# Optimization experiments

Hardware: AMD Instinct MI355X
Metric: run time of the kernel (lower is better)

Reference implementation:

```python
import jax, jax.numpy as jnp
import numpy as np

PRED_LEN = 6

def conv2d_same(x, w):
    # x: (B,H,W,Cin), w: (kh,kw,Cin,Cout) -> (B,H,W,Cout)
    return jax.lax.conv_general_dilated(
        x, w, window_strides=(1, 1), padding='SAME',
        dimension_numbers=('NHWC', 'HWIO', 'NHWC'))

def setup_inputs() -> dict:
    key = jax.random.key(0)
    ks = jax.random.split(key, 6)
    B, T, H, W, C = 8, 12, 128, 128, 1
    F = 64
    s_in = 1.0 / np.sqrt(3 * 3 * C)
    s_rec = 1.0 / np.sqrt(3 * 3 * F)
    return {
        'x': jax.random.normal(ks[0], (B, T, H, W, C), jnp.float32),
        'kernel': jax.random.normal(ks[1], (3, 3, C, 4 * F), jnp.float32) * s_in,
        'rec_kernel': jax.random.normal(ks[2], (3, 3, F, 4 * F), jnp.float32) * s_rec,
        'bias': jnp.zeros((4 * F,), jnp.float32),
        'w_out': jax.random.normal(ks[3], (3, 3, F, 1), jnp.float32) * s_rec,
        'b_out': jnp.zeros((1,), jnp.float32),
        'w_proj': jax.random.normal(ks[4], (1, 1, 1, F), jnp.float32),
        'b_proj': jnp.zeros((F,), jnp.float32),
    }

def reference(x, kernel, rec_kernel, bias, w_out, b_out, w_proj, b_proj):
    B, T, H, W, C = x.shape
    F = rec_kernel.shape[2]

    def step(carry, xt):
        h, c = carry
        # fused gate pre-activations: (B,H,W,4F), Keras gate order i,f,g,o
        z = conv2d_same(xt, kernel) + conv2d_same(h, rec_kernel) + bias
        i, f, g, o = jnp.split(z, 4, axis=-1)
        c_new = jax.nn.sigmoid(f) * c + jax.nn.sigmoid(i) * jnp.tanh(g)
        h_new = jax.nn.sigmoid(o) * jnp.tanh(c_new)
        return (h_new, c_new), None

    h0 = jnp.zeros((B, H, W, F), x.dtype)
    c0 = jnp.zeros((B, H, W, F), x.dtype)
    (h, c), _ = jax.lax.scan(step, (h0, c0), jnp.moveaxis(x, 1, 0))

    preds = []
    cur = h
    for _ in range(PRED_LEN):
        pred = jax.nn.sigmoid(conv2d_same(cur, w_out) + b_out)  # (B,H,W,1)
        preds.append(pred)
        cur = jax.nn.relu(conv2d_same(pred, w_proj) + b_proj)   # (B,H,W,F)
    return jnp.stack(preds, axis=1)  # (B,PRED_LEN,H,W,1)
```

## Files before the change

### kernel.cpp

```cpp
#include <hip/hip_runtime.h>
#include <math.h>

#define BB 8
#define TT 12
#define HH 128
#define WW 128
#define FF 64
#define GG 256
#define PRED_LEN 6
#define TW 64
#define TWD 32

typedef __attribute__((ext_vector_type(8))) short short8;
typedef __attribute__((ext_vector_type(4))) float floatx4;

__device__ __forceinline__ float sigf(float x) { return 1.f / (1.f + __expf(-x)); }
__device__ __forceinline__ float tanhfast(float x) { return 1.f - 2.f / (__expf(2.f * x) + 1.f); }

__device__ __forceinline__ unsigned short f2bf(float x) {
    unsigned u = __float_as_uint(x);
    u = (u + 0x7FFFu + ((u >> 16) & 1u)) >> 16;
    return (unsigned short)u;
}

__device__ __forceinline__ void decode_step(int wg, int& b, int& y, int& x0) {
    int lin = (wg & 7) * 128 + (wg >> 3);
    b = lin >> 7;
    int rem = lin & 127;
    y = (rem >> 1) * 2;
    x0 = (rem & 1) * TW;
}

__device__ __forceinline__ void decode_dec(int wg, int& b, int& y, int& x0) {
    int lin = (wg & 7) * 512 + (wg >> 3);
    b = lin >> 9;
    int rem = lin & 511;
    y = rem >> 2;
    x0 = (rem & 3) * TWD;
}

__global__ __launch_bounds__(256) void pack_wr(
    const float* __restrict__ wr, const float* __restrict__ wk,
    const float* __restrict__ bias, short8* __restrict__ packed)
{
    int e = blockIdx.x * 256 + threadIdx.x;
    if (e >= 19 * 16 * 64) return;
    int lane = e & 63;
    int rest = e >> 6;
    int nt = rest & 15;
    int ch = rest >> 4;
    int col = lane & 15, kpart = lane >> 4;
    int n = nt * 16 + col;
    short8 v;
    if (ch < 18) {
        int kc = ch & 1, tap = ch >> 1;
        #pragma unroll
        for (int j = 0; j < 8; ++j) {
            int k = kc * 32 + kpart * 8 + j;
            v[j] = (short)f2bf(wr[((size_t)(tap * 64 + k)) * GG + n]);
        }
    } else {
        #pragma unroll
        for (int j = 0; j < 8; ++j) {
            int k = kpart * 8 + j;
            unsigned short r = 0;
            if (k < 9) r = f2bf(wk[k * GG + n]);
            else if (k == 9) r = f2bf(bias[n]);
            v[j] = (short)r;
        }
    }
    packed[e] = v;
}

template<bool FIRST>
__global__ __launch_bounds__(512, 4) void lstm_step_mfma(
    const float* __restrict__ x,
    int t,
    const unsigned short* __restrict__ h_in,
    float* __restrict__ c_buf,
    unsigned short* __restrict__ h_out,
    const short8* __restrict__ packedB)
{
    __shared__ __align__(16) unsigned short sh[4 * 66 * FF];
    __shared__ __align__(16) unsigned short sxa[2][TW * 32];
    __shared__ float sx[4][66];

    const int tid = threadIdx.x;
    int b, y, x0;
    decode_step(blockIdx.x, b, y, x0);
    char* shb = (char*)sh;

    if (!FIRST) {
        for (int i = tid; i < 4 * 66 * 8; i += 512) {
            int cq  = i & 7;
            int rc  = i >> 3;
            int col = rc % 66, r = rc / 66;
            int gy = y + r - 1, gx = x0 + col - 1;
            uint4 v = make_uint4(0u, 0u, 0u, 0u);
            if ((unsigned)gy < HH && (unsigned)gx < WW)
                v = *(const uint4*)(h_in + ((((size_t)b * HH + gy) * WW + gx) * FF + cq * 8));
            int byte = ((r * 66 + col) * FF + cq * 8) * 2;
            byte ^= ((col & 7) << 4);
            *(uint4*)(shb + byte) = v;
        }
    }
    for (int i = tid; i < 4 * 66; i += 512) {
        int col = i % 66, r = i / 66;
        int gy = y + r - 1, gx = x0 + col - 1;
        float v = 0.f;
        if ((unsigned)gy < HH && (unsigned)gx < WW)
            v = x[(((size_t)b * TT + t) * HH + gy) * WW + gx];
        sx[r][col] = v;
    }
    __syncthreads();

    {
        int rr  = tid >> 8;
        int t2  = tid & 255;
        int px  = t2 >> 2, kpc = t2 & 3;
        short8 v;
        #pragma unroll
        for (int j = 0; j < 8; ++j) {
            int k = kpc * 8 + j;
            unsigned short r = 0;
            if (k < 9) r = f2bf(sx[rr + k / 3][px + (k % 3)]);
            else if (k == 9) r = (unsigned short)0x3F80;
            v[j] = (short)r;
        }
        int byte = (px * 64 + kpc * 16) ^ ((px & 7) << 4);
        *(short8*)((char*)sxa[rr] + byte) = v;
    }
    __syncthreads();

    const int l    = tid & 63;
    const int w    = tid >> 6;
    const int sw   = w & 3;
    const int rrow = w >> 2;
    const int lc = l & 15;
    const int kp = l >> 4;
    const int gcol = sw * 16 + lc;

    floatx4 acc[4][4];
    #pragma unroll
    for (int m = 0; m < 4; ++m)
        #pragma unroll
        for (int q = 0; q < 4; ++q)
            acc[m][q] = (floatx4){0.f, 0.f, 0.f, 0.f};

    if (!FIRST) {
        #pragma unroll
        for (int c = 0; c < 18; ++c) {
            const int tap_ = c >> 1, kc_ = c & 1, dy_ = tap_ / 3, dx_ = tap_ % 3;
            short8 af[4], bf[4];
            #pragma unroll
            for (int m_ = 0; m_ < 4; ++m_) {
                const int col_ = m_ * 16 + lc + dx_;
                int byte_ = (((dy_ + rrow) * 66 + col_) * FF + kc_ * 32 + kp * 8) * 2;
                byte_ ^= ((col_ & 7) << 4);
                af[m_] = *(const short8*)(shb + byte_);
            }
            #pragma unroll
            for (int q_ = 0; q_ < 4; ++q_)
                bf[q_] = packedB[(size_t)(c * 16 + (q_ * 4 + sw)) * 64 + l];
            #pragma unroll
            for (int m_ = 0; m_ < 4; ++m_)
                #pragma unroll
                for (int q_ = 0; q_ < 4; ++q_)
                    acc[m_][q_] = __builtin_amdgcn_mfma_f32_16x16x32_bf16(
                        af[m_], bf[q_], acc[m_][q_], 0, 0, 0);
        }
    }
    {
        short8 af[4], bf[4];
        #pragma unroll
        for (int m_ = 0; m_ < 4; ++m_) {
            const int px_ = m_ * 16 + lc;
            int byte_ = (px_ * 64 + kp * 16) ^ ((px_ & 7) << 4);
            af[m_] = *(const short8*)((const char*)sxa[rrow] + byte_);
        }
        #pragma unroll
        for (int q_ = 0; q_ < 4; ++q_)
            bf[q_] = packedB[(size_t)(18 * 16 + (q_ * 4 + sw)) * 64 + l];
        #pragma unroll
        for (int m_ = 0; m_ < 4; ++m_)
            #pragma unroll
            for (int q_ = 0; q_ < 4; ++q_)
                acc[m_][q_] = __builtin_amdgcn_mfma_f32_16x16x32_bf16(
                    af[m_], bf[q_], acc[m_][q_], 0, 0, 0);
    }

    #pragma unroll
    for (int m = 0; m < 4; ++m) {
        #pragma unroll
        for (int r = 0; r < 4; ++r) {
            int p = m * 16 + kp * 4 + r;
            size_t idx = (((size_t)b * HH + (y + rrow)) * WW + (x0 + p)) * FF + gcol;
            float cp = FIRST ? 0.f : c_buf[idx];
            float iv = sigf(acc[m][0][r]);
            float fv = sigf(acc[m][1][r]);
            float gv = tanhfast(acc[m][2][r]);
            float ov = sigf(acc[m][3][r]);
            float cn = fv * cp + iv * gv;
            float hn = ov * tanhfast(cn);
            c_buf[idx] = cn;
            h_out[idx] = f2bf(hn);
        }
    }
}

__global__ __launch_bounds__(256) void dec_fused(
    const unsigned short* __restrict__ cur_in, const float* __restrict__ w_out,
    const float* __restrict__ b_out, const float* __restrict__ w_proj,
    const float* __restrict__ b_proj, float* __restrict__ out,
    unsigned short* __restrict__ cur_out, int ti)
{
    int tid = threadIdx.x;
    int j  = tid & 7;
    int pp = tid >> 3;
    int b, y, x0;
    decode_dec(blockIdx.x, b, y, x0);
    int xx = x0 + pp;

    float s = 0.f;
    for (int dy = 0; dy < 3; ++dy) {
        int gy = y + dy - 1;
        if ((unsigned)gy >= HH) continue;
        #pragma unroll
        for (int dx = 0; dx < 3; ++dx) {
            int gx = xx + dx - 1;
            if ((unsigned)gx >= WW) continue;
            const uint4 cv = *(const uint4*)(cur_in + ((((size_t)b * HH + gy) * WW + gx) * FF + j * 8));
            const float4* wp = (const float4*)&w_out[(dy * 3 + dx) * FF + j * 8];
            float4 w0 = wp[0], w1 = wp[1];
            unsigned cx = cv.x, cy = cv.y, cz = cv.z, cw = cv.w;
            s += __uint_as_float(cx << 16) * w0.x + __uint_as_float(cx & 0xFFFF0000u) * w0.y
               + __uint_as_float(cy << 16) * w0.z + __uint_as_float(cy & 0xFFFF0000u) * w0.w
               + __uint_as_float(cz << 16) * w1.x + __uint_as_float(cz & 0xFFFF0000u) * w1.y
               + __uint_as_float(cw << 16) * w1.z + __uint_as_float(cw & 0xFFFF0000u) * w1.w;
        }
    }
    s += __shfl_xor(s, 1);
    s += __shfl_xor(s, 2);
    s += __shfl_xor(s, 4);
    float pv = sigf(s + b_out[0]);

    size_t pix = (((size_t)b * HH + y) * WW + xx);
    if (j == 0)
        out[((size_t)b * PRED_LEN + ti) * (HH * WW) + (size_t)y * WW + xx] = pv;

    const float4* wp = (const float4*)w_proj;
    const float4* bp = (const float4*)b_proj;
    float4 w0 = wp[j * 2], w1 = wp[j * 2 + 1];
    float4 b0 = bp[j * 2], b1 = bp[j * 2 + 1];
    short8 o;
    o[0] = (short)f2bf(fmaxf(fmaf(pv, w0.x, b0.x), 0.f));
    o[1] = (short)f2bf(fmaxf(fmaf(pv, w0.y, b0.y), 0.f));
    o[2] = (short)f2bf(fmaxf(fmaf(pv, w0.z, b0.z), 0.f));
    o[3] = (short)f2bf(fmaxf(fmaf(pv, w0.w, b0.w), 0.f));
    o[4] = (short)f2bf(fmaxf(fmaf(pv, w1.x, b1.x), 0.f));
    o[5] = (short)f2bf(fmaxf(fmaf(pv, w1.y, b1.y), 0.f));
    o[6] = (short)f2bf(fmaxf(fmaf(pv, w1.z, b1.z), 0.f));
    o[7] = (short)f2bf(fmaxf(fmaf(pv, w1.w, b1.w), 0.f));
    *(short8*)(cur_out + pix * FF + j * 8) = o;
}

extern "C" void kernel_launch(void* const* d_in, const int* in_sizes, int n_in,
                              void* d_out, int out_size, void* d_ws, size_t ws_size,
                              hipStream_t stream)
{
    const float* x      = (const float*)d_in[0];
    const float* wk     = (const float*)d_in[1];
    const float* wr     = (const float*)d_in[2];
    const float* bias   = (const float*)d_in[3];
    const float* w_out  = (const float*)d_in[4];
    const float* b_out  = (const float*)d_in[5];
    const float* w_proj = (const float*)d_in[6];
    const float* b_proj = (const float*)d_in[7];
    float* out = (float*)d_out;

    const size_t SB = (size_t)BB * HH * WW * FF;
    unsigned short* h_a = (unsigned short*)d_ws;
    unsigned short* h_b = h_a + SB;
    float* cb = (float*)((char*)d_ws + 2 * SB * sizeof(unsigned short));
    short8* packed = (short8*)((char*)cb + SB * sizeof(float));

    pack_wr<<<76, 256, 0, stream>>>(wr, wk, bias, packed);

    const int NBLK_STEP = (WW / TW) * (HH / 2) * BB;
    const int NBLK_DEC  = (WW / TWD) * HH * BB;
    unsigned short* bufs[2] = {h_a, h_b};
    lstm_step_mfma<true><<<NBLK_STEP, 512, 0, stream>>>(x, 0, bufs[0], cb, bufs[1], packed);
    for (int t = 1; t < TT; ++t) {
        lstm_step_mfma<false><<<NBLK_STEP, 512, 0, stream>>>(x, t, bufs[t & 1], cb,
                                                             bufs[(t + 1) & 1], packed);
    }

    for (int ti = 0; ti < PRED_LEN; ++ti) {
        dec_fused<<<NBLK_DEC, 256, 0, stream>>>(
            bufs[ti & 1], w_out, b_out, w_proj, b_proj, out, bufs[(ti + 1) & 1], ti);
    }
}
```

Before: 750.3 us.

## Stage packed weight fragments through LDS with double-buffered async global loads

Instead of each wave loading all B-operand weight fragments straight from global memory, the workgroup cooperatively loads each half-chunk of packed weights into a double-buffered LDS array with global_load_lds. The next chunk's load overlaps the current chunk's MFMAs. Each wave now issues one 16-byte load per step rather than four, so redundant global traffic drops. The cost is two workgroup barriers per half-chunk (38 iterations) and extra LDS use, which could limit occupancy at 4 blocks of 512 threads.

```diff
diff --git a/kernel.cpp b/kernel.cpp
--- a/kernel.cpp
+++ b/kernel.cpp
@@ -21,6 +21,13 @@
     unsigned u = __float_as_uint(x);
     u = (u + 0x7FFFu + ((u >> 16) & 1u)) >> 16;
     return (unsigned short)u;
+}
+
+__device__ __forceinline__ void gload_lds16(const void* g, void* l) {
+    __builtin_amdgcn_global_load_lds(
+        (const __attribute__((address_space(1))) unsigned int*)g,
+        (__attribute__((address_space(3))) unsigned int*)l,
+        16, 0, 0);
 }
 
 __device__ __forceinline__ void decode_step(int wg, int& b, int& y, int& x0) {
@@ -83,6 +90,7 @@
 {
     __shared__ __align__(16) unsigned short sh[4 * 66 * FF];
     __shared__ __align__(16) unsigned short sxa[2][TW * 32];
+    __shared__ __align__(16) short8 ldsB[2][8 * 64];
     __shared__ float sx[4][66];
 
     const int tid = threadIdx.x;
@@ -139,6 +147,7 @@
     const int lc = l & 15;
     const int kp = l >> 4;
     const int gcol = sw * 16 + lc;
+    const size_t base = (((size_t)b * HH + (y + rrow)) * WW + x0) * FF + gcol;
 
     floatx4 acc[4][4];
     #pragma unroll
@@ -147,46 +156,59 @@
         for (int q = 0; q < 4; ++q)
             acc[m][q] = (floatx4){0.f, 0.f, 0.f, 0.f};
 
-    if (!FIRST) {
-        #pragma unroll
-        for (int c = 0; c < 18; ++c) {
-            const int tap_ = c >> 1, kc_ = c & 1, dy_ = tap_ / 3, dx_ = tap_ % 3;
-            short8 af[4], bf[4];
-            #pragma unroll
-            for (int m_ = 0; m_ < 4; ++m_) {
-                const int col_ = m_ * 16 + lc + dx_;
-                int byte_ = (((dy_ + rrow) * 66 + col_) * FF + kc_ * 32 + kp * 8) * 2;
-                byte_ ^= ((col_ & 7) << 4);
-                af[m_] = *(const short8*)(shb + byte_);
+    constexpr int HC0 = FIRST ? 36 : 0;
+    {
+        constexpr int c1 = HC0 >> 1, h1 = HC0 & 1;
+        gload_lds16(packedB + ((size_t)(c1 * 16 + h1 * 8 + w) * 64 + l),
+                    &ldsB[HC0 & 1][w * 64]);
+    }
+    asm volatile("s_waitcnt vmcnt(0)" ::: "memory");
+    __builtin_amdgcn_s_barrier();
+    __builtin_amdgcn_sched_barrier(0);
+
+    short8 af[4];
+    #pragma unroll
+    for (int hc = HC0; hc < 38; ++hc) {
+        const int c = hc >> 1, half = hc & 1, buf = hc & 1;
+        if (hc + 1 < 38) {
+            const int c1 = (hc + 1) >> 1, h1 = (hc + 1) & 1;
+            gload_lds16(packedB + ((size_t)(c1 * 16 + h1 * 8 + w) * 64 + l),
+                        &ldsB[(hc + 1) & 1][w * 64]);
+            asm volatile("s_waitcnt vmcnt(1)" ::: "memory");
+        } else {
+            asm volatile("s_waitcnt vmcnt(0)" ::: "memory");
+        }
+        __builtin_amdgcn_s_barrier();
+        __builtin_amdgcn_sched_barrier(0);
+
+        if (half == 0) {
+            if (c < 18) {
+                const int tap_ = c >> 1, kc_ = c & 1, dy_ = tap_ / 3, dx_ = tap_ % 3;
+                #pragma unroll
+                for (int m_ = 0; m_ < 4; ++m_) {
+                    const int col_ = m_ * 16 + lc + dx_;
+                    int byte_ = (((dy_ + rrow) * 66 + col_) * FF + kc_ * 32 + kp * 8) * 2;
+                    byte_ ^= ((col_ & 7) << 4);
+                    af[m_] = *(const short8*)(shb + byte_);
+                }
+            } else {
+                #pragma unroll
+                for (int m_ = 0; m_ < 4; ++m_) {
+                    const int px_ = m_ * 16 + lc;
+                    int byte_ = (px_ * 64 + kp * 16) ^ ((px_ & 7) << 4);
+                    af[m_] = *(const short8*)((const char*)sxa[rrow] + byte_);
+                }
             }
-            #pragma unroll
-            for (int q_ = 0; q_ < 4; ++q_)
-                bf[q_] = packedB[(size_t)(c * 16 + (q_ * 4 + sw)) * 64 + l];
-            #pragma unroll
-            for (int m_ = 0; m_ < 4; ++m_)
-                #pragma unroll
-                for (int q_ = 0; q_ < 4; ++q_)
-                    acc[m_][q_] = __builtin_amdgcn_mfma_f32_16x16x32_bf16(
-                        af[m_], bf[q_], acc[m_][q_], 0, 0, 0);
-        }
-    }
-    {
-        short8 af[4], bf[4];
+        }
+        short8 bf0 = ldsB[buf][(0 + sw) * 64 + l];
+        short8 bf1 = ldsB[buf][(4 + sw) * 64 + l];
+        const int q0 = half * 2, q1 = half * 2 + 1;
         #pragma unroll
         for (int m_ = 0; m_ < 4; ++m_) {
-            const int px_ = m_ * 16 + lc;
-            int byte_ = (px_ * 64 + kp * 16) ^ ((px_ & 7) << 4);
-            af[m_] = *(const short8*)((const char*)sxa[rrow] + byte_);
-        }
-        #pragma unroll
-        for (int q_ = 0; q_ < 4; ++q_)
-            bf[q_] = packedB[(size_t)(18 * 16 + (q_ * 4 + sw)) * 64 + l];
-        #pragma unroll
-        for (int m_ = 0; m_ < 4; ++m_)
-            #pragma unroll
-            for (int q_ = 0; q_ < 4; ++q_)
-                acc[m_][q_] = __builtin_amdgcn_mfma_f32_16x16x32_bf16(
-                    af[m_], bf[q_], acc[m_][q_], 0, 0, 0);
+            acc[m_][q0] = __builtin_amdgcn_mfma_f32_16x16x32_bf16(af[m_], bf0, acc[m_][q0], 0, 0, 0);
+            acc[m_][q1] = __builtin_amdgcn_mfma_f32_16x16x32_bf16(af[m_], bf1, acc[m_][q1], 0, 0, 0);
+        }
+        __builtin_amdgcn_s_barrier();
     }
 
     #pragma unroll
@@ -194,13 +216,13 @@
         #pragma unroll
         for (int r = 0; r < 4; ++r) {
             int p = m * 16 + kp * 4 + r;
-            size_t idx = (((size_t)b * HH + (y + rrow)) * WW + (x0 + p)) * FF + gcol;
-            float cp = FIRST ? 0.f : c_buf[idx];
+            size_t idx = base + (size_t)p * FF;
+            float cpv = FIRST ? 0.f : c_buf[idx];
             float iv = sigf(acc[m][0][r]);
             float fv = sigf(acc[m][1][r]);
             float gv = tanhfast(acc[m][2][r]);
             float ov = sigf(acc[m][3][r]);
-            float cn = fv * cp + iv * gv;
+            float cn = fv * cpv + iv * gv;
             float hn = ov * tanhfast(cn);
             c_buf[idx] = cn;
             h_out[idx] = f2bf(hn);
```

Result: no change. 749.6 us (-0.1%).
